# Kernel optimization log

Hardware: AMD Instinct MI355X
Metric: run time of the kernel (lower is better)

Reference implementation:

```python
import jax, jax.numpy as jnp
import numpy as np

B, S, D, H, DK, DFF = 4, 1024, 1024, 16, 64, 4096
EPS = 1e-5


def layer_norm(x, g, b):
    m = jnp.mean(x, axis=-1, keepdims=True)
    v = jnp.var(x, axis=-1, keepdims=True)
    return (x - m) * jax.lax.rsqrt(v + EPS) * g + b


def setup_inputs() -> dict:
    key = jax.random.key(0)
    ks = jax.random.split(key, 12)
    sc = 0.02
    return {
        "x":    jax.random.normal(ks[0], (B, S, D), jnp.float32),
        # per-head Q/K/V projections, stacked over heads: [H, D, DK]
        "Wq":   jax.random.normal(ks[1], (H, D, DK), jnp.float32) * sc,
        "bq":   jnp.zeros((H, DK), jnp.float32),
        "Wk":   jax.random.normal(ks[2], (H, D, DK), jnp.float32) * sc,
        "bk":   jnp.zeros((H, DK), jnp.float32),
        "Wv":   jax.random.normal(ks[3], (H, D, DK), jnp.float32) * sc,
        "bv":   jnp.zeros((H, DK), jnp.float32),
        # output projection: [H*DK, D]
        "Wo":   jax.random.normal(ks[4], (H * DK, D), jnp.float32) * sc,
        "bo":   jnp.zeros((D,), jnp.float32),
        # FFN
        "W1":   jax.random.normal(ks[5], (D, DFF), jnp.float32) * sc,
        "b1":   jnp.zeros((DFF,), jnp.float32),
        "W2":   jax.random.normal(ks[6], (DFF, D), jnp.float32) * sc,
        "b2":   jnp.zeros((D,), jnp.float32),
        # LayerNorms
        "g1":   jnp.ones((D,), jnp.float32),
        "be1":  jnp.zeros((D,), jnp.float32),
        "g2":   jnp.ones((D,), jnp.float32),
        "be2":  jnp.zeros((D,), jnp.float32),
    }


def reference(x, Wq, bq, Wk, bk, Wv, bv, Wo, bo, W1, b1, W2, b2, g1, be1, g2, be2):
    # batched multi-head attention (original loops per head; math identical)
    q = jnp.einsum("bsd,hdk->bhsk", x, Wq) + bq[None, :, None, :]
    k = jnp.einsum("bsd,hdk->bhsk", x, Wk) + bk[None, :, None, :]
    v = jnp.einsum("bsd,hdk->bhsk", x, Wv) + bv[None, :, None, :]
    scale = 1.0 / jnp.sqrt(jnp.asarray(DK, x.dtype))
    scores = jnp.einsum("bhsk,bhtk->bhst", q * scale, k)
    attn = jax.nn.softmax(scores, axis=-1)  # dropout = eval-mode identity
    o = jnp.einsum("bhst,bhtk->bhsk", attn, v)
    # torch.cat over heads along dim 2 -> [B, S, H*DK]
    o = jnp.transpose(o, (0, 2, 1, 3)).reshape(B, S, H * DK)
    att = o @ Wo + bo
    # post-attn: residual of LayerNorm(att)
    x = x + layer_norm(att, g1, be1)
    # FFN
    pos = jax.nn.relu(x @ W1 + b1) @ W2 + b2
    x = x + layer_norm(pos, g2, be2)
    return x
```

## Files before the change

### kernel.cpp

```cpp
#include <hip/hip_runtime.h>
#include <hip/hip_bf16.h>

typedef unsigned short u16;
typedef short bf16x8_t __attribute__((ext_vector_type(8)));
typedef float f32x4_t  __attribute__((ext_vector_type(4)));

__device__ __forceinline__ u16 f2bf(float f) {
    __hip_bfloat16 h = __float2bfloat16(f);
    union { __hip_bfloat16 b; u16 u; } cv; cv.b = h; return cv.u;
}

__device__ __forceinline__ void g2l16(const void* g, void* l) {
    __builtin_amdgcn_global_load_lds(
        (const __attribute__((address_space(1))) unsigned int*)g,
        (__attribute__((address_space(3))) unsigned int*)l, 16, 0, 0);
}

__global__ __launch_bounds__(256) void k_cast_bf16v(const float* __restrict__ in,
                                                    u16* __restrict__ out, int n4) {
    int i = blockIdx.x * 256 + threadIdx.x;
    if (i < n4) {
        float4 f = ((const float4*)in)[i];
        ushort4 o;
        o.x = f2bf(f.x); o.y = f2bf(f.y); o.z = f2bf(f.z); o.w = f2bf(f.w);
        ((ushort4*)out)[i] = o;
    }
}

__global__ __launch_bounds__(256)
void k_transpose3(const float* __restrict__ Wo, const float* __restrict__ W1,
                  const float* __restrict__ W2, u16* __restrict__ Wot,
                  u16* __restrict__ W1t, u16* __restrict__ W2t) {
    int id = blockIdx.x;
    const float* in; u16* out; int R, C, tx, ty;
    if (id < 256)       { in = Wo; out = Wot; R = 1024; C = 1024; tx = id & 15; ty = id >> 4; }
    else if (id < 1280) { id -= 256; in = W1; out = W1t; R = 1024; C = 4096; tx = id & 63; ty = id >> 6; }
    else                { id -= 1280; in = W2; out = W2t; R = 4096; C = 1024; tx = id & 15; ty = id >> 4; }
    __shared__ float t[64][65];
    int r0 = ty * 64, c0 = tx * 64;
    int lc = threadIdx.x & 63, lr = threadIdx.x >> 6;
#pragma unroll
    for (int p = 0; p < 16; ++p) {
        int rr = p * 4 + lr;
        t[rr][lc] = in[(size_t)(r0 + rr) * C + c0 + lc];
    }
    __syncthreads();
#pragma unroll
    for (int p = 0; p < 16; ++p) {
        int cc = p * 4 + lr;
        out[(size_t)(c0 + cc) * R + r0 + lc] = f2bf(t[lc][cc]);
    }
}

__global__ __launch_bounds__(256)
void k_qkvw_t(const float* __restrict__ Wq, const float* __restrict__ Wk,
              const float* __restrict__ Wv, u16* __restrict__ out) {
    const float* in = blockIdx.z == 0 ? Wq : (blockIdx.z == 1 ? Wk : Wv);
    in += (size_t)blockIdx.y * 65536;
    u16* o = out + ((size_t)blockIdx.z * 1024 + blockIdx.y * 64) * 1024;
    __shared__ float t[64][65];
    int d0 = blockIdx.x * 64;
    int lc = threadIdx.x & 63, lr = threadIdx.x >> 6;
#pragma unroll
    for (int p = 0; p < 16; ++p) {
        int rr = p * 4 + lr;
        t[rr][lc] = in[(size_t)(d0 + rr) * 64 + lc];
    }
    __syncthreads();
#pragma unroll
    for (int p = 0; p < 16; ++p) {
        int cc = p * 4 + lr;
        o[(size_t)cc * 1024 + d0 + lc] = f2bf(t[lc][cc]);
    }
}

__global__ __launch_bounds__(256)
void k_vt(const u16* __restrict__ V, u16* __restrict__ VT) {
    __shared__ u16 t[64 * 72];
    int bh = blockIdx.y, s0 = blockIdx.x * 64;
    const u16* Vp = V + (size_t)bh * 65536;
    u16* Tp = VT + (size_t)bh * 65536;
    int tid = threadIdx.x;
    int r = tid >> 3, c = (tid & 7) * 8;
    *(uint4*)&t[r * 72 + c]        = *(const uint4*)&Vp[(size_t)(s0 + r) * 64 + c];
    *(uint4*)&t[(r + 32) * 72 + c] = *(const uint4*)&Vp[(size_t)(s0 + r + 32) * 64 + c];
    __syncthreads();
    int d = tid >> 2, sl0 = (tid & 3) * 16;
    uint4 outv[2];
    u16* ov = (u16*)outv;
#pragma unroll
    for (int j = 0; j < 16; ++j) ov[j] = t[(sl0 + j) * 72 + d];
    *(uint4*)&Tp[(size_t)d * 1024 + s0 + sl0]     = outv[0];
    *(uint4*)&Tp[(size_t)d * 1024 + s0 + sl0 + 8] = outv[1];
}

template<int EPI>
__global__ __launch_bounds__(256, 4)
void k_gemm_bt(const u16* __restrict__ A, const u16* __restrict__ Bt,
               const float* __restrict__ bias0, void* __restrict__ out,
               int M, int N, int K, int kchunk)
{
    __shared__ __align__(16) u16 As[2 * 128 * 32];
    __shared__ __align__(16) u16 Bs[2 * 128 * 32];
    int tid = threadIdx.x;
    int wave = tid >> 6, lane = tid & 63;

    int nx = gridDim.x, nwg = nx * gridDim.y;
    int f  = blockIdx.x + nx * blockIdx.y;
    int f2 = (f & 7) * (nwg >> 3) + (f >> 3);
    int bx = f2 % nx, by = f2 / nx;
    int row0 = by * 128, col0 = bx * 128;

    int z = blockIdx.z;
    int kbeg = z * kchunk;

    int lrow = lane >> 2, lcol = (lane & 3) * 8;
    const u16* pA0 = A  + (size_t)(row0 + wave * 16 + lrow) * K + kbeg + lcol;
    const u16* pA1 = pA0 + (size_t)64 * K;
    const u16* pB0 = Bt + (size_t)(col0 + wave * 16 + lrow) * K + kbeg + lcol;
    const u16* pB1 = pB0 + (size_t)64 * K;
    u16* lA0 = &As[wave * 512];
    u16* lA1 = &As[2048 + wave * 512];
    u16* lB0 = &Bs[wave * 512];
    u16* lB1 = &Bs[2048 + wave * 512];

    int wm = (wave >> 1) * 64, wn = (wave & 1) * 64;
    int quad = lane >> 4, l16 = lane & 15;

    f32x4_t acc[4][4];
#pragma unroll
    for (int i = 0; i < 4; i++)
#pragma unroll
        for (int j = 0; j < 4; j++) acc[i][j] = f32x4_t{0.f, 0.f, 0.f, 0.f};

    for (int kk = 0; kk < kchunk; kk += 64) {
        __syncthreads();
        g2l16(pA0, lA0);      g2l16(pA1, lA1);
        g2l16(pA0 + 32, lA0 + 4096); g2l16(pA1 + 32, lA1 + 4096);
        g2l16(pB0, lB0);      g2l16(pB1, lB1);
        g2l16(pB0 + 32, lB0 + 4096); g2l16(pB1 + 32, lB1 + 4096);
        pA0 += 64; pA1 += 64; pB0 += 64; pB1 += 64;
        __syncthreads();

#pragma unroll
        for (int s = 0; s < 2; ++s) {
            const u16* as = &As[s * 4096];
            const u16* bs = &Bs[s * 4096];
            bf16x8_t a[4], b[4];
#pragma unroll
            for (int i = 0; i < 4; ++i)
                a[i] = *(const bf16x8_t*)&as[(wm + i * 16 + l16) * 32 + quad * 8];
#pragma unroll
            for (int j = 0; j < 4; ++j)
                b[j] = *(const bf16x8_t*)&bs[(wn + j * 16 + l16) * 32 + quad * 8];
#pragma unroll
            for (int i = 0; i < 4; ++i)
#pragma unroll
                for (int j = 0; j < 4; ++j)
                    acc[i][j] = __builtin_amdgcn_mfma_f32_16x16x32_bf16(a[i], b[j], acc[i][j], 0, 0, 0);
        }
    }

#pragma unroll
    for (int i = 0; i < 4; ++i)
#pragma unroll
        for (int j = 0; j < 4; ++j)
#pragma unroll
            for (int r = 0; r < 4; ++r) {
                int row = row0 + wm + i * 16 + quad * 4 + r;
                int col = col0 + wn + j * 16 + l16;
                ((float*)out)[(size_t)z * M * N + (size_t)row * N + col] = acc[i][j][r];
            }
}

template<int EPI>
__global__ __launch_bounds__(512, 4)
void k_gemm_bt2(const u16* __restrict__ A, const u16* __restrict__ Bt,
                const float* __restrict__ bias0, const float* __restrict__ bias1,
                const float* __restrict__ bias2, void* __restrict__ out,
                int M, int N, int K)
{
    __shared__ __align__(16) u16 As[2 * 256 * 32];
    __shared__ __align__(16) u16 Bs[2 * 128 * 32];
    int tid = threadIdx.x;
    int wave = tid >> 6, lane = tid & 63;
    int row0 = blockIdx.y * 256, col0 = blockIdx.x * 128;

    int lrow = lane >> 2, lcol = (lane & 3) * 8;
    const u16* pA0 = A  + (size_t)(row0 + wave * 16 + lrow) * K + lcol;
    const u16* pA1 = pA0 + (size_t)128 * K;
    const u16* pB0 = Bt + (size_t)(col0 + wave * 16 + lrow) * K + lcol;
    u16* lA0 = &As[wave * 512];
    u16* lA1 = &As[4096 + wave * 512];
    u16* lB0 = &Bs[wave * 512];

    int wm = (wave >> 1) * 64, wn = (wave & 1) * 64;
    int quad = lane >> 4, l16 = lane & 15;

    f32x4_t acc[4][4];
#pragma unroll
    for (int i = 0; i < 4; i++)
#pragma unroll
        for (int j = 0; j < 4; j++) acc[i][j] = f32x4_t{0.f, 0.f, 0.f, 0.f};

    for (int kk = 0; kk < K; kk += 64) {
        __syncthreads();
        g2l16(pA0, lA0);           g2l16(pA1, lA1);
        g2l16(pA0 + 32, lA0 + 8192); g2l16(pA1 + 32, lA1 + 8192);
        g2l16(pB0, lB0);           g2l16(pB0 + 32, lB0 + 4096);
        pA0 += 64; pA1 += 64; pB0 += 64;
        __syncthreads();

#pragma unroll
        for (int s = 0; s < 2; ++s) {
            const u16* as = &As[s * 8192];
            const u16* bs = &Bs[s * 4096];
            bf16x8_t a[4], b[4];
#pragma unroll
            for (int i = 0; i < 4; ++i)
                a[i] = *(const bf16x8_t*)&as[(wm + i * 16 + l16) * 32 + quad * 8];
#pragma unroll
            for (int j = 0; j < 4; ++j)
                b[j] = *(const bf16x8_t*)&bs[(wn + j * 16 + l16) * 32 + quad * 8];
#pragma unroll
            for (int i = 0; i < 4; ++i)
#pragma unroll
                for (int j = 0; j < 4; ++j)
                    acc[i][j] = __builtin_amdgcn_mfma_f32_16x16x32_bf16(a[i], b[j], acc[i][j], 0, 0, 0);
        }
    }

#pragma unroll
    for (int i = 0; i < 4; ++i)
#pragma unroll
        for (int j = 0; j < 4; ++j)
#pragma unroll
            for (int r = 0; r < 4; ++r) {
                int row = row0 + wm + i * 16 + quad * 4 + r;
                int col = col0 + wn + j * 16 + l16;
                float v = acc[i][j][r];
                if (EPI == 1) {
                    ((u16*)out)[(size_t)row * N + col] = f2bf(fmaxf(v + bias0[col], 0.f));
                } else {
                    int proj = col >> 10, within = col & 1023;
                    const float* bp = proj == 0 ? bias0 : (proj == 1 ? bias1 : bias2);
                    v += bp[within];
                    if (proj == 0) v *= 0.18033688f;
                    int h = within >> 6, kq = within & 63;
                    int b_ = row >> 10, s_ = row & 1023;
                    size_t bh = (size_t)((b_ << 4) + h);
                    ((u16*)out)[(size_t)proj * 4194304 + bh * 65536 + (s_ << 6) + kq] = f2bf(v);
                }
            }
}

__global__ __launch_bounds__(512, 4)
void k_attn(const u16* __restrict__ Qg, const u16* __restrict__ Kg,
            const u16* __restrict__ VTg, u16* __restrict__ Og)
{
    __shared__ __align__(16) u16 Ks[64 * 64];
    __shared__ __align__(16) u16 Vs[64 * 64];
    __shared__ __align__(16) u16 Ps[128 * 64];

    int tid = threadIdx.x, wave = tid >> 6, lane = tid & 63;
    int quad = lane >> 4, l16 = lane & 15;

    int f  = blockIdx.x + gridDim.x * blockIdx.y;
    int f2 = (f & 7) * ((gridDim.x * gridDim.y) >> 3) + (f >> 3);
    int bh = f2 >> 3;
    int q0 = (f2 & 7) * 128;
    int wrow = wave * 16;

    const u16* Qp  = Qg  + (size_t)bh * 65536;
    const u16* Kp  = Kg  + (size_t)bh * 65536;
    const u16* VTp = VTg + (size_t)bh * 65536;

    int arow_g = q0 + wrow + l16;
    bf16x8_t aq0 = *(const bf16x8_t*)&Qp[(size_t)arow_g * 64 + quad * 8];
    bf16x8_t aq1 = *(const bf16x8_t*)&Qp[(size_t)arow_g * 64 + 32 + quad * 8];

    int srow = tid >> 3, scb = tid & 7;
    uint4 kreg = *(const uint4*)&Kp[(size_t)srow * 64 + scb * 8];
    uint4 vreg = *(const uint4*)&VTp[(size_t)srow * 1024 + scb * 8];
    u16* kdst = &Ks[srow * 64 + ((scb ^ (srow & 7)) * 8)];
    u16* vdst = &Vs[srow * 64 + ((scb ^ (srow & 7)) * 8)];

    f32x4_t o[4], lsum;
#pragma unroll
    for (int nt = 0; nt < 4; ++nt) o[nt] = f32x4_t{0.f, 0.f, 0.f, 0.f};
    lsum = f32x4_t{0.f, 0.f, 0.f, 0.f};

    bf16x8_t ones;
#pragma unroll
    for (int j = 0; j < 8; ++j) ones[j] = (short)0x3F80;

    int a7 = l16 & 7;

    for (int kv0 = 0; kv0 < 1024; kv0 += 64) {
        __syncthreads();
        *(uint4*)kdst = kreg;
        *(uint4*)vdst = vreg;
        __syncthreads();
        if (kv0 < 960) {
            kreg = *(const uint4*)&Kp[(size_t)(kv0 + 64 + srow) * 64 + scb * 8];
            vreg = *(const uint4*)&VTp[(size_t)srow * 1024 + kv0 + 64 + scb * 8];
        }

        f32x4_t s[4];
#pragma unroll
        for (int nt = 0; nt < 4; ++nt) {
            int brow = nt * 16 + l16;
            bf16x8_t bk0 = *(const bf16x8_t*)&Ks[brow * 64 + ((quad ^ a7) * 8)];
            bf16x8_t bk1 = *(const bf16x8_t*)&Ks[brow * 64 + (((4 + quad) ^ a7) * 8)];
            s[nt] = __builtin_amdgcn_mfma_f32_16x16x32_bf16(aq0, bk0, f32x4_t{0.f,0.f,0.f,0.f}, 0, 0, 0);
            s[nt] = __builtin_amdgcn_mfma_f32_16x16x32_bf16(aq1, bk1, s[nt], 0, 0, 0);
        }

#pragma unroll
        for (int nt = 0; nt < 4; ++nt) {
            int pcb = nt * 2 + (l16 >> 3);
#pragma unroll
            for (int r = 0; r < 4; ++r) {
                float p = exp2f(s[nt][r]);
                int pr = wrow + quad * 4 + r;
                Ps[pr * 64 + ((pcb ^ (pr & 7)) * 8) + (l16 & 7)] = f2bf(p);
            }
        }

        int arow = wrow + l16;
        bf16x8_t ap0 = *(const bf16x8_t*)&Ps[arow * 64 + ((quad ^ a7) * 8)];
        bf16x8_t ap1 = *(const bf16x8_t*)&Ps[arow * 64 + (((4 + quad) ^ a7) * 8)];
#pragma unroll
        for (int nt = 0; nt < 4; ++nt) {
            int vrow = nt * 16 + l16;
            bf16x8_t bv0 = *(const bf16x8_t*)&Vs[vrow * 64 + ((quad ^ a7) * 8)];
            bf16x8_t bv1 = *(const bf16x8_t*)&Vs[vrow * 64 + (((4 + quad) ^ a7) * 8)];
            o[nt] = __builtin_amdgcn_mfma_f32_16x16x32_bf16(ap0, bv0, o[nt], 0, 0, 0);
            o[nt] = __builtin_amdgcn_mfma_f32_16x16x32_bf16(ap1, bv1, o[nt], 0, 0, 0);
        }
        lsum = __builtin_amdgcn_mfma_f32_16x16x32_bf16(ap0, ones, lsum, 0, 0, 0);
        lsum = __builtin_amdgcn_mfma_f32_16x16x32_bf16(ap1, ones, lsum, 0, 0, 0);
    }

    int b = bh >> 4, h = bh & 15;
    float invl[4];
#pragma unroll
    for (int r = 0; r < 4; ++r) invl[r] = 1.f / lsum[r];
#pragma unroll
    for (int nt = 0; nt < 4; ++nt)
#pragma unroll
        for (int r = 0; r < 4; ++r) {
            int srow2 = q0 + wrow + quad * 4 + r;
            Og[(size_t)(b * 1024 + srow2) * 1024 + (h << 6) + nt * 16 + l16] = f2bf(o[nt][r] * invl[r]);
        }
}

template<int MODE, int NP>
__global__ __launch_bounds__(256)
void k_ln2(const float* __restrict__ p, const float* __restrict__ bias,
           const float* __restrict__ residf, const u16* __restrict__ residb,
           const float* __restrict__ g, const float* __restrict__ be,
           float* __restrict__ out, u16* __restrict__ outb)
{
    int row = blockIdx.x, tid = threadIdx.x;
    size_t base = (size_t)row * 1024;
    float xv[4]; float s = 0.f, sq = 0.f;
#pragma unroll
    for (int i = 0; i < 4; i++) {
        int c = tid + i * 256;
        float t = bias[c];
#pragma unroll
        for (int z = 0; z < NP; ++z) t += p[(size_t)z * 4194304 + base + c];
        xv[i] = t;
        s += t; sq += t * t;
    }
#pragma unroll
    for (int off = 32; off; off >>= 1) { s += __shfl_down(s, off); sq += __shfl_down(sq, off); }
    __shared__ float ss[4], ssq[4];
    int wv = tid >> 6;
    if ((tid & 63) == 0) { ss[wv] = s; ssq[wv] = sq; }
    __syncthreads();
    s  = ss[0] + ss[1] + ss[2] + ss[3];
    sq = ssq[0] + ssq[1] + ssq[2] + ssq[3];
    float mean = s * (1.f / 1024.f);
    float var  = sq * (1.f / 1024.f) - mean * mean;
    float rstd = rsqrtf(var + 1e-5f);
#pragma unroll
    for (int i = 0; i < 4; i++) {
        int c = tid + i * 256;
        float rv;
        if (MODE == 0) rv = residf[base + c];
        else {
            union { u16 u[2]; unsigned int w; float f; } cv;
            cv.w = (unsigned int)residb[base + c] << 16;
            rv = cv.f;
        }
        float y = rv + (xv[i] - mean) * rstd * g[c] + be[c];
        if (MODE == 0) outb[base + c] = f2bf(y);
        else           out[base + c] = y;
    }
}

extern "C" void kernel_launch(void* const* d_in, const int* in_sizes, int n_in,
                              void* d_out, int out_size, void* d_ws, size_t ws_size,
                              hipStream_t stream) {
    const float* x   = (const float*)d_in[0];
    const float* Wq  = (const float*)d_in[1];
    const float* bq  = (const float*)d_in[2];
    const float* Wk  = (const float*)d_in[3];
    const float* bk  = (const float*)d_in[4];
    const float* Wv  = (const float*)d_in[5];
    const float* bv  = (const float*)d_in[6];
    const float* Wo  = (const float*)d_in[7];
    const float* bo  = (const float*)d_in[8];
    const float* W1  = (const float*)d_in[9];
    const float* b1  = (const float*)d_in[10];
    const float* W2  = (const float*)d_in[11];
    const float* b2  = (const float*)d_in[12];
    const float* g1  = (const float*)d_in[13];
    const float* be1 = (const float*)d_in[14];
    const float* g2  = (const float*)d_in[15];
    const float* be2 = (const float*)d_in[16];
    float* out = (float*)d_out;

    char* w = (char*)d_ws;
    u16*   Xb    = (u16*)(w);
    u16*   VTb   = (u16*)(w);
    u16*   Wqkvt = (u16*)(w + 8388608);
    u16*   Wot   = (u16*)(w + 14680064);
    u16*   W1t   = (u16*)(w + 16777216);
    u16*   W2t   = (u16*)(w + 25165824);
    u16*   Qb    = (u16*)(w + 33554432);
    u16*   Kb    = (u16*)(w + 41943040);
    u16*   Vb    = (u16*)(w + 50331648);
    u16*   Oc    = (u16*)(w + 58720256);
    float* part2 = (float*)(w + 67108864);
    float* part4 = (float*)(w + 33554432);
    u16*   x1b   = (u16*)(w + 117440512);
    u16*   hb    = (u16*)(w + 125829120);

    k_cast_bf16v<<<4096, 256, 0, stream>>>(x, Xb, 1048576);
    k_qkvw_t<<<dim3(16, 16, 3), 256, 0, stream>>>(Wq, Wk, Wv, Wqkvt);
    k_transpose3<<<2304, 256, 0, stream>>>(Wo, W1, W2, Wot, W1t, W2t);

    k_gemm_bt2<2><<<dim3(24, 16), 512, 0, stream>>>(Xb, Wqkvt, bq, bk, bv, Qb, 4096, 3072, 1024);

    k_vt<<<dim3(16, 64), 256, 0, stream>>>(Vb, VTb);

    k_attn<<<dim3(8, 64), 512, 0, stream>>>(Qb, Kb, VTb, Oc);

    k_gemm_bt<0><<<dim3(8, 32, 2), 256, 0, stream>>>(Oc, Wot, nullptr, part2, 4096, 1024, 1024, 512);

    k_ln2<0, 2><<<4096, 256, 0, stream>>>(part2, bo, x, nullptr, g1, be1, nullptr, x1b);

    k_gemm_bt2<1><<<dim3(32, 16), 512, 0, stream>>>(x1b, W1t, b1, nullptr, nullptr, hb, 4096, 4096, 1024);

    k_gemm_bt<0><<<dim3(8, 32, 4), 256, 0, stream>>>(hb, W2t, nullptr, part4, 4096, 1024, 4096, 1024);

    k_ln2<1, 4><<<4096, 256, 0, stream>>>(part4, b2, nullptr, x1b, g2, be2, out, nullptr);
}
```

Measured before the change: 323.9 us.

## Replace GEMM kernel with 256x256-tile pipelined kernel using swizzled LDS and split-K

Replaces the 256x128-tile GEMM with a new 256x256-tile kernel. It double-buffers LDS loads staged across four MFMA phases, uses an XOR-swizzled LDS layout to avoid bank conflicts, raises MFMA priority with setprio, and remaps workgroups for locality. The QKV, FFN1 and FFN2 GEMMs now use it, FFN2 through a split-K epilogue. Larger tiles increase data reuse and overlap loads with compute, at the cost of more registers and LDS per block and lower occupancy.

```diff
diff --git a/kernel.cpp b/kernel.cpp
--- a/kernel.cpp
+++ b/kernel.cpp
@@ -174,72 +174,142 @@
 }
 
 template<int EPI>
-__global__ __launch_bounds__(512, 4)
-void k_gemm_bt2(const u16* __restrict__ A, const u16* __restrict__ Bt,
-                const float* __restrict__ bias0, const float* __restrict__ bias1,
-                const float* __restrict__ bias2, void* __restrict__ out,
-                int M, int N, int K)
+__global__ __launch_bounds__(512, 2)
+void k_gemm8(const u16* __restrict__ A, const u16* __restrict__ Bt,
+             const float* __restrict__ bias0, const float* __restrict__ bias1,
+             const float* __restrict__ bias2, void* __restrict__ out,
+             int M, int N, int K, int kchunk)
 {
-    __shared__ __align__(16) u16 As[2 * 256 * 32];
-    __shared__ __align__(16) u16 Bs[2 * 128 * 32];
-    int tid = threadIdx.x;
-    int wave = tid >> 6, lane = tid & 63;
-    int row0 = blockIdx.y * 256, col0 = blockIdx.x * 128;
-
-    int lrow = lane >> 2, lcol = (lane & 3) * 8;
-    const u16* pA0 = A  + (size_t)(row0 + wave * 16 + lrow) * K + lcol;
-    const u16* pA1 = pA0 + (size_t)128 * K;
-    const u16* pB0 = Bt + (size_t)(col0 + wave * 16 + lrow) * K + lcol;
-    u16* lA0 = &As[wave * 512];
-    u16* lA1 = &As[4096 + wave * 512];
-    u16* lB0 = &Bs[wave * 512];
-
-    int wm = (wave >> 1) * 64, wn = (wave & 1) * 64;
-    int quad = lane >> 4, l16 = lane & 15;
-
-    f32x4_t acc[4][4];
-#pragma unroll
-    for (int i = 0; i < 4; i++)
-#pragma unroll
-        for (int j = 0; j < 4; j++) acc[i][j] = f32x4_t{0.f, 0.f, 0.f, 0.f};
-
-    for (int kk = 0; kk < K; kk += 64) {
-        __syncthreads();
-        g2l16(pA0, lA0);           g2l16(pA1, lA1);
-        g2l16(pA0 + 32, lA0 + 8192); g2l16(pA1 + 32, lA1 + 8192);
-        g2l16(pB0, lB0);           g2l16(pB0 + 32, lB0 + 4096);
-        pA0 += 64; pA1 += 64; pB0 += 64;
-        __syncthreads();
-
-#pragma unroll
-        for (int s = 0; s < 2; ++s) {
-            const u16* as = &As[s * 8192];
-            const u16* bs = &Bs[s * 4096];
-            bf16x8_t a[4], b[4];
-#pragma unroll
-            for (int i = 0; i < 4; ++i)
-                a[i] = *(const bf16x8_t*)&as[(wm + i * 16 + l16) * 32 + quad * 8];
-#pragma unroll
-            for (int j = 0; j < 4; ++j)
-                b[j] = *(const bf16x8_t*)&bs[(wn + j * 16 + l16) * 32 + quad * 8];
-#pragma unroll
-            for (int i = 0; i < 4; ++i)
-#pragma unroll
-                for (int j = 0; j < 4; ++j)
-                    acc[i][j] = __builtin_amdgcn_mfma_f32_16x16x32_bf16(a[i], b[j], acc[i][j], 0, 0, 0);
-        }
-    }
-
-#pragma unroll
-    for (int i = 0; i < 4; ++i)
-#pragma unroll
-        for (int j = 0; j < 4; ++j)
+    __shared__ __align__(16) u16 As[2][16384];
+    __shared__ __align__(16) u16 Bs[2][16384];
+
+    const int tid = threadIdx.x;
+    const int wave = tid >> 6, lane = tid & 63;
+    const int quad = lane >> 4, l16 = lane & 15;
+    const int wm = (wave >> 2) * 128;
+    const int wn = (wave & 3) * 64;
+
+    int nx = gridDim.x, nwg = nx * gridDim.y;
+    int f  = blockIdx.x + nx * blockIdx.y;
+    int f2 = (f & 7) * (nwg >> 3) + (f >> 3);
+    int row0 = (f2 / nx) * 256, col0 = (f2 % nx) * 256;
+    int z = blockIdx.z, kbeg = z * kchunk;
+    int nk = kchunk >> 6;
+
+    const int rr0 = tid >> 3, cg = tid & 7;
+    const int xc = (cg ^ (rr0 & 7)) * 8;
+    const u16* Ag = A  + (size_t)(row0 + rr0) * K + kbeg + xc;
+    const u16* Bg = Bt + (size_t)(col0 + rr0) * K + kbeg + xc;
+    const int ldst = tid * 8;
+
+#define STA(bsel, h, kt) do { \
+    const u16* _s = Ag + (size_t)(h) * 128 * K + (size_t)(kt) * 64; \
+    g2l16(_s, &As[bsel][(h) * 8192 + ldst]); \
+    g2l16(_s + (size_t)64 * K, &As[bsel][(h) * 8192 + 4096 + ldst]); } while (0)
+#define STB(bsel, h, kt) do { \
+    const u16* _s = Bg + (size_t)(h) * 128 * K + (size_t)(kt) * 64; \
+    g2l16(_s, &Bs[bsel][(h) * 8192 + ldst]); \
+    g2l16(_s + (size_t)64 * K, &Bs[bsel][(h) * 8192 + 4096 + ldst]); } while (0)
+
+#define RDA(b, mi, ks) (*(const bf16x8_t*)&As[b][(wm + (mi) * 16 + l16) * 64 + ((((ks) * 4 + quad) ^ (l16 & 7)) * 8)])
+#define RDB(b, nj, ks) (*(const bf16x8_t*)&Bs[b][(wn + (nj) * 16 + l16) * 64 + ((((ks) * 4 + quad) ^ (l16 & 7)) * 8)])
+
+    f32x4_t acc[8][4];
+#pragma unroll
+    for (int i = 0; i < 8; ++i)
+#pragma unroll
+        for (int j = 0; j < 4; ++j) acc[i][j] = f32x4_t{0.f, 0.f, 0.f, 0.f};
+
+    STA(0, 0, 0); STA(0, 1, 0); STB(0, 0, 0); STB(0, 1, 0);
+    if (nk > 1) {
+        STB(1, 0, 1); STB(1, 1, 1);
+        asm volatile("s_waitcnt vmcnt(4)" ::: "memory");
+    } else {
+        asm volatile("s_waitcnt vmcnt(0)" ::: "memory");
+    }
+    __builtin_amdgcn_s_barrier();
+
+    bf16x8_t av[4][2], bv0[2][2], bv1[2][2];
+    for (int t = 0; t < nk; ++t) {
+        int b = t & 1, bn = b ^ 1;
+#pragma unroll
+        for (int i = 0; i < 4; ++i) { av[i][0] = RDA(b, i, 0); av[i][1] = RDA(b, i, 1); }
+#pragma unroll
+        for (int j = 0; j < 2; ++j) { bv0[j][0] = RDB(b, j, 0); bv0[j][1] = RDB(b, j, 1); }
+        if (t + 1 < nk) STA(bn, 0, t + 1);
+        __builtin_amdgcn_s_barrier();
+        __builtin_amdgcn_s_setprio(1);
+#pragma unroll
+        for (int i = 0; i < 4; ++i)
+#pragma unroll
+            for (int j = 0; j < 2; ++j) {
+                acc[i][j] = __builtin_amdgcn_mfma_f32_16x16x32_bf16(av[i][0], bv0[j][0], acc[i][j], 0, 0, 0);
+                acc[i][j] = __builtin_amdgcn_mfma_f32_16x16x32_bf16(av[i][1], bv0[j][1], acc[i][j], 0, 0, 0);
+            }
+        __builtin_amdgcn_s_setprio(0);
+        __builtin_amdgcn_s_barrier();
+#pragma unroll
+        for (int j = 0; j < 2; ++j) { bv1[j][0] = RDB(b, 2 + j, 0); bv1[j][1] = RDB(b, 2 + j, 1); }
+        if (t + 1 < nk) STA(bn, 1, t + 1);
+        __builtin_amdgcn_s_barrier();
+        __builtin_amdgcn_s_setprio(1);
+#pragma unroll
+        for (int i = 0; i < 4; ++i)
+#pragma unroll
+            for (int j = 0; j < 2; ++j) {
+                acc[i][2 + j] = __builtin_amdgcn_mfma_f32_16x16x32_bf16(av[i][0], bv1[j][0], acc[i][2 + j], 0, 0, 0);
+                acc[i][2 + j] = __builtin_amdgcn_mfma_f32_16x16x32_bf16(av[i][1], bv1[j][1], acc[i][2 + j], 0, 0, 0);
+            }
+        __builtin_amdgcn_s_setprio(0);
+        __builtin_amdgcn_s_barrier();
+#pragma unroll
+        for (int i = 0; i < 4; ++i) { av[i][0] = RDA(b, 4 + i, 0); av[i][1] = RDA(b, 4 + i, 1); }
+        if (t + 2 < nk) STB(b, 0, t + 2);
+        __builtin_amdgcn_s_barrier();
+        __builtin_amdgcn_s_setprio(1);
+#pragma unroll
+        for (int i = 0; i < 4; ++i)
+#pragma unroll
+            for (int j = 0; j < 2; ++j) {
+                acc[4 + i][j] = __builtin_amdgcn_mfma_f32_16x16x32_bf16(av[i][0], bv0[j][0], acc[4 + i][j], 0, 0, 0);
+                acc[4 + i][j] = __builtin_amdgcn_mfma_f32_16x16x32_bf16(av[i][1], bv0[j][1], acc[4 + i][j], 0, 0, 0);
+            }
+        __builtin_amdgcn_s_setprio(0);
+        __builtin_amdgcn_s_barrier();
+        if (t + 2 < nk) STB(b, 1, t + 2);
+        __builtin_amdgcn_s_barrier();
+        __builtin_amdgcn_s_setprio(1);
+#pragma unroll
+        for (int i = 0; i < 4; ++i)
+#pragma unroll
+            for (int j = 0; j < 2; ++j) {
+                acc[4 + i][2 + j] = __builtin_amdgcn_mfma_f32_16x16x32_bf16(av[i][0], bv1[j][0], acc[4 + i][2 + j], 0, 0, 0);
+                acc[4 + i][2 + j] = __builtin_amdgcn_mfma_f32_16x16x32_bf16(av[i][1], bv1[j][1], acc[4 + i][2 + j], 0, 0, 0);
+            }
+        __builtin_amdgcn_s_setprio(0);
+        if (t + 1 < nk) {
+            if (t + 2 < nk) asm volatile("s_waitcnt vmcnt(4)" ::: "memory");
+            else            asm volatile("s_waitcnt vmcnt(0)" ::: "memory");
+        }
+        __builtin_amdgcn_s_barrier();
+    }
+#undef STA
+#undef STB
+#undef RDA
+#undef RDB
+
+#pragma unroll
+    for (int mi = 0; mi < 8; ++mi)
+#pragma unroll
+        for (int nj = 0; nj < 4; ++nj)
 #pragma unroll
             for (int r = 0; r < 4; ++r) {
-                int row = row0 + wm + i * 16 + quad * 4 + r;
-                int col = col0 + wn + j * 16 + l16;
-                float v = acc[i][j][r];
-                if (EPI == 1) {
+                int row = row0 + wm + mi * 16 + quad * 4 + r;
+                int col = col0 + wn + nj * 16 + l16;
+                float v = acc[mi][nj][r];
+                if (EPI == 0) {
+                    ((float*)out)[(size_t)z * M * N + (size_t)row * N + col] = v;
+                } else if (EPI == 1) {
                     ((u16*)out)[(size_t)row * N + col] = f2bf(fmaxf(v + bias0[col], 0.f));
                 } else {
                     int proj = col >> 10, within = col & 1023;
@@ -443,7 +513,7 @@
     k_qkvw_t<<<dim3(16, 16, 3), 256, 0, stream>>>(Wq, Wk, Wv, Wqkvt);
     k_transpose3<<<2304, 256, 0, stream>>>(Wo, W1, W2, Wot, W1t, W2t);
 
-    k_gemm_bt2<2><<<dim3(24, 16), 512, 0, stream>>>(Xb, Wqkvt, bq, bk, bv, Qb, 4096, 3072, 1024);
+    k_gemm8<2><<<dim3(12, 16), 512, 0, stream>>>(Xb, Wqkvt, bq, bk, bv, Qb, 4096, 3072, 1024, 1024);
 
     k_vt<<<dim3(16, 64), 256, 0, stream>>>(Vb, VTb);
 
@@ -453,9 +523,9 @@
 
     k_ln2<0, 2><<<4096, 256, 0, stream>>>(part2, bo, x, nullptr, g1, be1, nullptr, x1b);
 
-    k_gemm_bt2<1><<<dim3(32, 16), 512, 0, stream>>>(x1b, W1t, b1, nullptr, nullptr, hb, 4096, 4096, 1024);
-
-    k_gemm_bt<0><<<dim3(8, 32, 4), 256, 0, stream>>>(hb, W2t, nullptr, part4, 4096, 1024, 4096, 1024);
+    k_gemm8<1><<<dim3(16, 16), 512, 0, stream>>>(x1b, W1t, b1, nullptr, nullptr, hb, 4096, 4096, 1024, 1024);
+
+    k_gemm8<0><<<dim3(4, 16, 4), 512, 0, stream>>>(hb, W2t, nullptr, nullptr, nullptr, part4, 4096, 1024, 4096, 1024);
 
     k_ln2<1, 4><<<4096, 256, 0, stream>>>(part4, b2, nullptr, x1b, g2, be2, out, nullptr);
 }
```

After: 326.4 us. No clear change (+0.8%).

## Store split-K partials in fp16 and merge prep kernels into one launch

Applied to the files above, without the earlier changes.

The split-K GEMM partial sums for the output projection and FFN down-projection are now stored as fp16 instead of fp32, and the layernorm kernels read and convert them. This halves the write and read traffic of the partial buffers. Separately, the input cast and the three weight transpose kernels are merged into one prep launch to cut launch overhead. The fp16 partials lose precision and could overflow on large values.

```diff
diff --git a/kernel.cpp b/kernel.cpp
--- a/kernel.cpp
+++ b/kernel.cpp
@@ -1,5 +1,6 @@
 #include <hip/hip_runtime.h>
 #include <hip/hip_bf16.h>
+#include <hip/hip_fp16.h>
 
 typedef unsigned short u16;
 typedef short bf16x8_t __attribute__((ext_vector_type(8)));
@@ -16,28 +17,39 @@
         (__attribute__((address_space(3))) unsigned int*)l, 16, 0, 0);
 }
 
-__global__ __launch_bounds__(256) void k_cast_bf16v(const float* __restrict__ in,
-                                                    u16* __restrict__ out, int n4) {
-    int i = blockIdx.x * 256 + threadIdx.x;
-    if (i < n4) {
-        float4 f = ((const float4*)in)[i];
+__global__ __launch_bounds__(256)
+void k_prep(const float* __restrict__ x, u16* __restrict__ Xb,
+            const float* __restrict__ Wq, const float* __restrict__ Wk,
+            const float* __restrict__ Wv, u16* __restrict__ Wqkvt,
+            const float* __restrict__ Wo, const float* __restrict__ W1,
+            const float* __restrict__ W2, u16* __restrict__ Wot,
+            u16* __restrict__ W1t, u16* __restrict__ W2t)
+{
+    int id = blockIdx.x;
+    if (id < 4096) {
+        int i = id * 256 + threadIdx.x;
+        float4 f = ((const float4*)x)[i];
         ushort4 o;
         o.x = f2bf(f.x); o.y = f2bf(f.y); o.z = f2bf(f.z); o.w = f2bf(f.w);
-        ((ushort4*)out)[i] = o;
-    }
-}
-
-__global__ __launch_bounds__(256)
-void k_transpose3(const float* __restrict__ Wo, const float* __restrict__ W1,
-                  const float* __restrict__ W2, u16* __restrict__ Wot,
-                  u16* __restrict__ W1t, u16* __restrict__ W2t) {
-    int id = blockIdx.x;
-    const float* in; u16* out; int R, C, tx, ty;
-    if (id < 256)       { in = Wo; out = Wot; R = 1024; C = 1024; tx = id & 15; ty = id >> 4; }
-    else if (id < 1280) { id -= 256; in = W1; out = W1t; R = 1024; C = 4096; tx = id & 63; ty = id >> 6; }
-    else                { id -= 1280; in = W2; out = W2t; R = 4096; C = 1024; tx = id & 15; ty = id >> 4; }
+        ((ushort4*)Xb)[i] = o;
+        return;
+    }
+    id -= 4096;
+    const float* in; u16* out; int R, C, r0, c0;
+    if (id < 768) {
+        int zx = id >> 8, hy = (id >> 4) & 15, tx = id & 15;
+        in  = (zx == 0 ? Wq : (zx == 1 ? Wk : Wv)) + (size_t)hy * 65536;
+        out = Wqkvt + ((size_t)zx * 1024 + hy * 64) * 1024;
+        R = 1024; C = 64; r0 = tx * 64; c0 = 0;
+    } else {
+        id -= 768;
+        int tx, ty;
+        if (id < 256)       { in = Wo; out = Wot; R = 1024; C = 1024; tx = id & 15; ty = id >> 4; }
+        else if (id < 1280) { id -= 256; in = W1; out = W1t; R = 1024; C = 4096; tx = id & 63; ty = id >> 6; }
+        else                { id -= 1280; in = W2; out = W2t; R = 4096; C = 1024; tx = id & 15; ty = id >> 4; }
+        r0 = ty * 64; c0 = tx * 64;
+    }
     __shared__ float t[64][65];
-    int r0 = ty * 64, c0 = tx * 64;
     int lc = threadIdx.x & 63, lr = threadIdx.x >> 6;
 #pragma unroll
     for (int p = 0; p < 16; ++p) {
@@ -49,28 +61,6 @@
     for (int p = 0; p < 16; ++p) {
         int cc = p * 4 + lr;
         out[(size_t)(c0 + cc) * R + r0 + lc] = f2bf(t[lc][cc]);
-    }
-}
-
-__global__ __launch_bounds__(256)
-void k_qkvw_t(const float* __restrict__ Wq, const float* __restrict__ Wk,
-              const float* __restrict__ Wv, u16* __restrict__ out) {
-    const float* in = blockIdx.z == 0 ? Wq : (blockIdx.z == 1 ? Wk : Wv);
-    in += (size_t)blockIdx.y * 65536;
-    u16* o = out + ((size_t)blockIdx.z * 1024 + blockIdx.y * 64) * 1024;
-    __shared__ float t[64][65];
-    int d0 = blockIdx.x * 64;
-    int lc = threadIdx.x & 63, lr = threadIdx.x >> 6;
-#pragma unroll
-    for (int p = 0; p < 16; ++p) {
-        int rr = p * 4 + lr;
-        t[rr][lc] = in[(size_t)(d0 + rr) * 64 + lc];
-    }
-    __syncthreads();
-#pragma unroll
-    for (int p = 0; p < 16; ++p) {
-        int cc = p * 4 + lr;
-        o[(size_t)cc * 1024 + d0 + lc] = f2bf(t[lc][cc]);
     }
 }
 
@@ -94,11 +84,9 @@
     *(uint4*)&Tp[(size_t)d * 1024 + s0 + sl0 + 8] = outv[1];
 }
 
-template<int EPI>
 __global__ __launch_bounds__(256, 4)
 void k_gemm_bt(const u16* __restrict__ A, const u16* __restrict__ Bt,
-               const float* __restrict__ bias0, void* __restrict__ out,
-               int M, int N, int K, int kchunk)
+               void* __restrict__ out, int M, int N, int K, int kchunk)
 {
     __shared__ __align__(16) u16 As[2 * 128 * 32];
     __shared__ __align__(16) u16 Bs[2 * 128 * 32];
@@ -169,7 +157,8 @@
             for (int r = 0; r < 4; ++r) {
                 int row = row0 + wm + i * 16 + quad * 4 + r;
                 int col = col0 + wn + j * 16 + l16;
-                ((float*)out)[(size_t)z * M * N + (size_t)row * N + col] = acc[i][j][r];
+                ((__half*)out)[(size_t)z * M * N + (size_t)row * N + col] =
+                    __float2half(acc[i][j][r]);
             }
 }
 
@@ -357,7 +346,7 @@
 
 template<int MODE, int NP>
 __global__ __launch_bounds__(256)
-void k_ln2(const float* __restrict__ p, const float* __restrict__ bias,
+void k_ln2(const __half* __restrict__ p, const float* __restrict__ bias,
            const float* __restrict__ residf, const u16* __restrict__ residb,
            const float* __restrict__ g, const float* __restrict__ be,
            float* __restrict__ out, u16* __restrict__ outb)
@@ -370,7 +359,7 @@
         int c = tid + i * 256;
         float t = bias[c];
 #pragma unroll
-        for (int z = 0; z < NP; ++z) t += p[(size_t)z * 4194304 + base + c];
+        for (int z = 0; z < NP; ++z) t += __half2float(p[(size_t)z * 4194304 + base + c]);
         xv[i] = t;
         s += t; sq += t * t;
     }
@@ -424,24 +413,22 @@
     float* out = (float*)d_out;
 
     char* w = (char*)d_ws;
-    u16*   Xb    = (u16*)(w);
-    u16*   VTb   = (u16*)(w);
-    u16*   Wqkvt = (u16*)(w + 8388608);
-    u16*   Wot   = (u16*)(w + 14680064);
-    u16*   W1t   = (u16*)(w + 16777216);
-    u16*   W2t   = (u16*)(w + 25165824);
-    u16*   Qb    = (u16*)(w + 33554432);
-    u16*   Kb    = (u16*)(w + 41943040);
-    u16*   Vb    = (u16*)(w + 50331648);
-    u16*   Oc    = (u16*)(w + 58720256);
-    float* part2 = (float*)(w + 67108864);
-    float* part4 = (float*)(w + 33554432);
-    u16*   x1b   = (u16*)(w + 117440512);
-    u16*   hb    = (u16*)(w + 125829120);
-
-    k_cast_bf16v<<<4096, 256, 0, stream>>>(x, Xb, 1048576);
-    k_qkvw_t<<<dim3(16, 16, 3), 256, 0, stream>>>(Wq, Wk, Wv, Wqkvt);
-    k_transpose3<<<2304, 256, 0, stream>>>(Wo, W1, W2, Wot, W1t, W2t);
+    u16*    Xb    = (u16*)(w);
+    u16*    VTb   = (u16*)(w);
+    u16*    Wqkvt = (u16*)(w + 8388608);
+    u16*    Wot   = (u16*)(w + 14680064);
+    u16*    W1t   = (u16*)(w + 16777216);
+    u16*    W2t   = (u16*)(w + 25165824);
+    u16*    Qb    = (u16*)(w + 33554432);
+    u16*    Kb    = (u16*)(w + 41943040);
+    u16*    Vb    = (u16*)(w + 50331648);
+    u16*    Oc    = (u16*)(w + 58720256);
+    __half* part4 = (__half*)(w + 33554432);
+    __half* part2 = (__half*)(w + 67108864);
+    u16*    x1b   = (u16*)(w + 117440512);
+    u16*    hb    = (u16*)(w + 125829120);
+
+    k_prep<<<7168, 256, 0, stream>>>(x, Xb, Wq, Wk, Wv, Wqkvt, Wo, W1, W2, Wot, W1t, W2t);
 
     k_gemm_bt2<2><<<dim3(24, 16), 512, 0, stream>>>(Xb, Wqkvt, bq, bk, bv, Qb, 4096, 3072, 1024);
 
@@ -449,13 +436,13 @@
 
     k_attn<<<dim3(8, 64), 512, 0, stream>>>(Qb, Kb, VTb, Oc);
 
-    k_gemm_bt<0><<<dim3(8, 32, 2), 256, 0, stream>>>(Oc, Wot, nullptr, part2, 4096, 1024, 1024, 512);
+    k_gemm_bt<<<dim3(8, 32, 2), 256, 0, stream>>>(Oc, Wot, part2, 4096, 1024, 1024, 512);
 
     k_ln2<0, 2><<<4096, 256, 0, stream>>>(part2, bo, x, nullptr, g1, be1, nullptr, x1b);
 
     k_gemm_bt2<1><<<dim3(32, 16), 512, 0, stream>>>(x1b, W1t, b1, nullptr, nullptr, hb, 4096, 4096, 1024);
 
-    k_gemm_bt<0><<<dim3(8, 32, 4), 256, 0, stream>>>(hb, W2t, nullptr, part4, 4096, 1024, 4096, 1024);
+    k_gemm_bt<<<dim3(8, 32, 4), 256, 0, stream>>>(hb, W2t, part4, 4096, 1024, 4096, 1024);
 
     k_ln2<1, 4><<<4096, 256, 0, stream>>>(part4, b2, nullptr, x1b, g2, be2, out, nullptr);
 }
```

New measurement: 308.4 us. 1.05x faster.
